# Performance work log

Hardware: AMD Instinct MI355X
Metric: run time of the kernel (lower is better)

## Reference

```python
import jax, jax.numpy as jnp
import numpy as np

DIM, HEADS, WIN, MLP_H = 768, 12, 14, 3072
B, H0, W0 = 8, 64, 64
N = H0 * W0
SCALE = (DIM // HEADS) ** -0.5
EPS = 1e-5


def setup_inputs():
    key = jax.random.key(0)
    ks = jax.random.split(key, 8)
    w = lambda k, shape: jax.random.normal(k, shape, jnp.float32) * 0.02
    return {
        "x": jax.random.normal(ks[0], (B, N, DIM), jnp.float32),
        "rel_pos_bias": jax.random.normal(ks[1], (HEADS, WIN * WIN, WIN * WIN), jnp.float32) * 0.1,
        "ln1_g": jnp.ones((DIM,), jnp.float32),
        "ln1_b": jnp.zeros((DIM,), jnp.float32),
        "qkv_w": w(ks[2], (3 * DIM, DIM)),
        "qkv_b": jnp.zeros((3 * DIM,), jnp.float32),
        "proj_w": w(ks[3], (DIM, DIM)),
        "proj_b": jnp.zeros((DIM,), jnp.float32),
        "ln2_g": jnp.ones((DIM,), jnp.float32),
        "ln2_b": jnp.zeros((DIM,), jnp.float32),
        "fc1_w": w(ks[4], (MLP_H, DIM)),
        "fc1_b": jnp.zeros((MLP_H,), jnp.float32),
        "fc2_w": w(ks[5], (DIM, MLP_H)),
        "fc2_b": jnp.zeros((DIM,), jnp.float32),
        "H": H0,
        "W": W0,
    }


def layernorm(x, g, b):
    m = x.mean(-1, keepdims=True)
    v = ((x - m) ** 2).mean(-1, keepdims=True)
    return (x - m) / jnp.sqrt(v + EPS) * g + b


def make_window(x, H, W, win):
    Bc, _, C = x.shape
    x = x.reshape(Bc, H, W, C)
    ph, pw = (-H) % win, (-W) % win
    x = jnp.pad(x, ((0, 0), (0, ph), (0, pw), (0, 0)))
    Hp, Wp = H + ph, W + pw
    x = x.reshape(Bc, Hp // win, win, Wp // win, win, C)
    x = x.transpose(0, 1, 3, 2, 4, 5).reshape(-1, win * win, C)
    return x, Hp, Wp


def revert_window(x, Hp, Wp, H, W, win):
    Bc = x.shape[0] // ((Hp // win) * (Wp // win))
    C = x.shape[-1]
    x = x.reshape(Bc, Hp // win, Wp // win, win, win, C)
    x = x.transpose(0, 1, 3, 2, 4, 5).reshape(Bc, Hp, Wp, C)
    return x[:, :H, :W, :].reshape(Bc, H * W, C)


def attention(x, rel_pos_bias, qkv_w, qkv_b, proj_w, proj_b):
    Bw, Nw, C = x.shape
    dh = C // HEADS
    qkv = (x @ qkv_w.T + qkv_b).reshape(Bw, Nw, 3, HEADS, dh)
    q, k, v = (qkv[:, :, i].transpose(0, 2, 1, 3) for i in range(3))  # [Bw, h, Nw, dh]
    attn = jnp.einsum("bhqd,bhkd->bhqk", q, k) * SCALE + rel_pos_bias[None]
    attn = jax.nn.softmax(attn, axis=-1)
    out = jnp.einsum("bhqk,bhkd->bhqd", attn, v)
    out = out.transpose(0, 2, 1, 3).reshape(Bw, Nw, C)
    return out @ proj_w.T + proj_b


def reference(x, rel_pos_bias, ln1_g, ln1_b, qkv_w, qkv_b, proj_w, proj_b,
              ln2_g, ln2_b, fc1_w, fc1_b, fc2_w, fc2_b, H, W):
    ori = x
    h = layernorm(x, ln1_g, ln1_b)
    hw, Hp, Wp = make_window(h, H, W, WIN)
    hw = attention(hw, rel_pos_bias, qkv_w, qkv_b, proj_w, proj_b)
    h = revert_window(hw, Hp, Wp, H, W, WIN)
    x = ori + h
    m = layernorm(x, ln2_g, ln2_b)
    m = jax.nn.gelu(m @ fc1_w.T + fc1_b, approximate=False) @ fc2_w.T + fc2_b
    return x + m
```

## Files before the change

### kernel.cpp

```cpp
#include <hip/hip_runtime.h>


typedef unsigned short u16;
typedef unsigned int u32;
typedef __attribute__((ext_vector_type(4))) float f32x4;
typedef __attribute__((ext_vector_type(8))) __bf16 bf16x8;

#define DIMC 768
#define HEADS 12
#define WIN2 196
#define MLP_H 3072
#define MW 39200
#define MWPAD 39296
#define HW_ROWS 39312
#define MM 32768

__device__ __forceinline__ u16 f2bf(float f) {
  u32 u = __float_as_uint(f);
  u32 r = (u + 0x7fffu + ((u >> 16) & 1u)) >> 16;
  return (u16)r;
}

__device__ __forceinline__ f32x4 mfma16(bf16x8 a, bf16x8 b, f32x4 c) {
  return __builtin_amdgcn_mfma_f32_16x16x32_bf16(a, b, c, 0, 0, 0);
}

__device__ __forceinline__ void gload_lds16(const u16* g, u16* l) {
  __builtin_amdgcn_global_load_lds((__attribute__((address_space(1))) void*)g,
                                   (__attribute__((address_space(3))) void*)l,
                                   16, 0, 0);
}

__global__ __launch_bounds__(256) void cvt_bf16(const float* __restrict__ s,
                                                u16* __restrict__ d, int n) {
  for (int i = blockIdx.x * 256 + threadIdx.x; i < n; i += gridDim.x * 256)
    d[i] = f2bf(s[i]);
}

__global__ __launch_bounds__(256) void ln1_win_kernel(const float* __restrict__ x,
    const float* __restrict__ g, const float* __restrict__ bb,
    u16* __restrict__ hw) {
  int row = blockIdx.x;
  int t = threadIdx.x;
  const float* src = nullptr;
  if (row < MW) {
    int w = row / WIN2, p = row % WIN2;
    int b = w / 25, wi = w % 25;
    int wy = wi / 5, wx = wi % 5;
    int yy = wy * 14 + p / 14, xx = wx * 14 + p % 14;
    if (yy < 64 && xx < 64) src = x + ((size_t)b * 4096 + (size_t)yy * 64 + xx) * DIMC;
  }
  u16* dst = hw + (size_t)row * DIMC;
  if (src == nullptr) {
    for (int i = t; i < DIMC; i += 256) dst[i] = 0;
    return;
  }
  float v0 = src[t], v1 = src[t + 256], v2 = src[t + 512];
  __shared__ float red[8];
  float s = v0 + v1 + v2;
#pragma unroll
  for (int o = 32; o >= 1; o >>= 1) s += __shfl_xor(s, o);
  if ((t & 63) == 0) red[t >> 6] = s;
  __syncthreads();
  float mean = (red[0] + red[1] + red[2] + red[3]) * (1.0f / 768.0f);
  float d0 = v0 - mean, d1 = v1 - mean, d2 = v2 - mean;
  float q = d0 * d0 + d1 * d1 + d2 * d2;
#pragma unroll
  for (int o = 32; o >= 1; o >>= 1) q += __shfl_xor(q, o);
  if ((t & 63) == 0) red[4 + (t >> 6)] = q;
  __syncthreads();
  float var = (red[4] + red[5] + red[6] + red[7]) * (1.0f / 768.0f);
  float rstd = rsqrtf(var + 1e-5f);
  dst[t]       = f2bf(d0 * rstd * g[t]       + bb[t]);
  dst[t + 256] = f2bf(d1 * rstd * g[t + 256] + bb[t + 256]);
  dst[t + 512] = f2bf(d2 * rstd * g[t + 512] + bb[t + 512]);
}

__global__ __launch_bounds__(256) void ln_kernel(const float* __restrict__ x,
    const float* __restrict__ g, const float* __restrict__ bb,
    u16* __restrict__ out) {
  int row = blockIdx.x;
  int t = threadIdx.x;
  const float* src = x + (size_t)row * DIMC;
  u16* dst = out + (size_t)row * DIMC;
  float v0 = src[t], v1 = src[t + 256], v2 = src[t + 512];
  __shared__ float red[8];
  float s = v0 + v1 + v2;
#pragma unroll
  for (int o = 32; o >= 1; o >>= 1) s += __shfl_xor(s, o);
  if ((t & 63) == 0) red[t >> 6] = s;
  __syncthreads();
  float mean = (red[0] + red[1] + red[2] + red[3]) * (1.0f / 768.0f);
  float d0 = v0 - mean, d1 = v1 - mean, d2 = v2 - mean;
  float q = d0 * d0 + d1 * d1 + d2 * d2;
#pragma unroll
  for (int o = 32; o >= 1; o >>= 1) q += __shfl_xor(q, o);
  if ((t & 63) == 0) red[4 + (t >> 6)] = q;
  __syncthreads();
  float var = (red[4] + red[5] + red[6] + red[7]) * (1.0f / 768.0f);
  float rstd = rsqrtf(var + 1e-5f);
  dst[t]       = f2bf(d0 * rstd * g[t]       + bb[t]);
  dst[t + 256] = f2bf(d1 * rstd * g[t + 256] + bb[t + 256]);
  dst[t + 512] = f2bf(d2 * rstd * g[t + 512] + bb[t + 512]);
}

template <int EPI>
__global__ __launch_bounds__(256) void gemm_bt(
    const u16* __restrict__ A, const u16* __restrict__ W,
    const float* __restrict__ bias, int K, int N,
    u16* __restrict__ outb, float* __restrict__ outf,
    const float* __restrict__ resid) {
  __shared__ u16 As[128 * 32];
  __shared__ u16 Bs[128 * 32];
  int tid = threadIdx.x, lane = tid & 63, wv = tid >> 6;
  int bm = blockIdx.x, bn = blockIdx.y;
  int wr = wv >> 1, wc = wv & 1;
  const int fq = lane >> 4, fr = lane & 15;

  f32x4 acc[4][4];
#pragma unroll
  for (int m = 0; m < 4; ++m)
#pragma unroll
    for (int n = 0; n < 4; ++n) acc[m][n] = f32x4{0.f, 0.f, 0.f, 0.f};

  int nk = K >> 5;
  for (int kt = 0; kt < nk; ++kt) {
#pragma unroll
    for (int s2 = 0; s2 < 2; ++s2) {
      int seg = wv * 2 + s2;
      int ci = seg * 64 + lane;
      int rowIn = ci >> 2;
      int kch = (ci & 3) ^ (rowIn & 3);
      const u16* ga = A + (size_t)(bm * 128 + rowIn) * K + kt * 32 + kch * 8;
      gload_lds16(ga, &As[seg * 512]);
      const u16* gb = W + (size_t)(bn * 128 + rowIn) * K + kt * 32 + kch * 8;
      gload_lds16(gb, &Bs[seg * 512]);
    }
    __syncthreads();
    bf16x8 af[4], bfr[4];
#pragma unroll
    for (int m = 0; m < 4; ++m) {
      int row = wr * 64 + m * 16 + fr;
      int kch = fq ^ (row & 3);
      af[m] = *(const bf16x8*)&As[row * 32 + kch * 8];
    }
#pragma unroll
    for (int n = 0; n < 4; ++n) {
      int row = wc * 64 + n * 16 + fr;
      int kch = fq ^ (row & 3);
      bfr[n] = *(const bf16x8*)&Bs[row * 32 + kch * 8];
    }
#pragma unroll
    for (int m = 0; m < 4; ++m)
#pragma unroll
      for (int n = 0; n < 4; ++n)
        acc[m][n] = mfma16(af[m], bfr[n], acc[m][n]);
    __syncthreads();
  }

  float bcol[4];
#pragma unroll
  for (int n = 0; n < 4; ++n) bcol[n] = bias[bn * 128 + wc * 64 + n * 16 + fr];

#pragma unroll
  for (int m = 0; m < 4; ++m) {
#pragma unroll
    for (int j = 0; j < 4; ++j) {
      int row = bm * 128 + wr * 64 + m * 16 + fq * 4 + j;
#pragma unroll
      for (int n = 0; n < 4; ++n) {
        int col = bn * 128 + wc * 64 + n * 16 + fr;
        float v = acc[m][n][j] + bcol[n];
        if constexpr (EPI == 0) {
          outb[(size_t)row * N + col] = f2bf(v);
        } else if constexpr (EPI == 2) {
          v = 0.5f * v * (1.0f + erff(v * 0.70710678118654752f));
          outb[(size_t)row * N + col] = f2bf(v);
        } else if constexpr (EPI == 1) {
          if (row < MW) {
            int w = row / WIN2, p = row % WIN2;
            int b = w / 25, wi = w % 25;
            int yy = (wi / 5) * 14 + p / 14, xx = (wi % 5) * 14 + p % 14;
            if (yy < 64 && xx < 64) {
              size_t o = ((size_t)b * 4096 + (size_t)yy * 64 + xx) * DIMC + col;
              outf[o] = resid[o] + v;
            }
          }
        } else {
          size_t o = (size_t)row * DIMC + col;
          outf[o] = resid[o] + v;
        }
      }
    }
  }
}

#define ATTN_LDS 94208
__global__ __launch_bounds__(256) void attn_kernel(const u16* __restrict__ qkv,
    const float* __restrict__ bias, u16* __restrict__ aout) {
  extern __shared__ char smem[];
  int tid = threadIdx.x, lane = tid & 63, wv = tid >> 6;
  int blk = blockIdx.x;
  int w = blk / HEADS, h = blk % HEADS;
  const size_t rbase = (size_t)w * WIN2;
  char* KsB = smem;
  char* VtB = smem + 28672;
  char* PsB = smem + 61440 + wv * 8192;

  for (int c = tid; c < 1792; c += 256) {
    int row = c >> 3, off = (c & 7) << 4;
    char* d = KsB + row * 128 + (off ^ ((row & 7) << 4));
    if (row < WIN2) {
      const u16* gp = qkv + (rbase + row) * 2304 + 768 + h * 64 + (off >> 1);
      *(uint4*)d = *(const uint4*)gp;
    } else {
      *(uint4*)d = make_uint4(0u, 0u, 0u, 0u);
    }
  }
  for (int c = tid; c < 1792; c += 256) {
    int row = c >> 3, d0 = (c & 7) << 3;
    u16 tmp[8];
    if (row < WIN2) {
      const u16* gp = qkv + (rbase + row) * 2304 + 1536 + h * 64 + d0;
#pragma unroll
      for (int i = 0; i < 8; ++i) tmp[i] = gp[i];
    } else {
#pragma unroll
      for (int i = 0; i < 8; ++i) tmp[i] = 0;
    }
#pragma unroll
    for (int i = 0; i < 8; ++i) {
      int dd = d0 + i;
      int k2 = row << 1;
      *(u16*)(VtB + dd * 512 + (k2 ^ ((dd & 7) << 4))) = tmp[i];
    }
  }
  __syncthreads();

  const int fq = lane >> 4, fr = lane & 15;
  for (int qt = wv; qt < 13; qt += 4) {
    int qrow = qt * 16 + fr;
    if (qrow > 195) qrow = 195;
    const u16* qg = qkv + (rbase + qrow) * 2304 + h * 64 + fq * 8;
    bf16x8 qa0 = *(const bf16x8*)qg;
    bf16x8 qa1 = *(const bf16x8*)(qg + 32);

    f32x4 sacc[14];
#pragma unroll
    for (int ct = 0; ct < 14; ++ct) {
      int krow = ct * 16 + fr;
      const char* kp = KsB + krow * 128;
      bf16x8 kb0 = *(const bf16x8*)(kp + ((fq * 16) ^ ((krow & 7) << 4)));
      bf16x8 kb1 = *(const bf16x8*)(kp + ((64 + fq * 16) ^ ((krow & 7) << 4)));
      f32x4 z = f32x4{0.f, 0.f, 0.f, 0.f};
      z = mfma16(qa0, kb0, z);
      z = mfma16(qa1, kb1, z);
      sacc[ct] = z;
    }

    int qb = qt * 16 + fq * 4;
    float rs[4];
#pragma unroll
    for (int j = 0; j < 4; ++j) {
      int q = qb + j;
      int qc = q > 195 ? 195 : q;
      const float* bp = bias + ((size_t)h * WIN2 + qc) * WIN2;
      float mx = -1e30f;
#pragma unroll
      for (int ct = 0; ct < 14; ++ct) {
        int kc = ct * 16 + fr;
        float sv = (kc < WIN2) ? sacc[ct][j] * 0.125f + bp[kc] : -1e30f;
        sacc[ct][j] = sv;
        mx = fmaxf(mx, sv);
      }
#pragma unroll
      for (int o = 1; o < 16; o <<= 1) mx = fmaxf(mx, __shfl_xor(mx, o));
      float sum = 0.f;
#pragma unroll
      for (int ct = 0; ct < 14; ++ct) {
        float p = __expf(sacc[ct][j] - mx);
        sacc[ct][j] = p;
        sum += p;
      }
#pragma unroll
      for (int o = 1; o < 16; o <<= 1) sum += __shfl_xor(sum, o);
      rs[j] = sum;
    }

#pragma unroll
    for (int ct = 0; ct < 14; ++ct) {
#pragma unroll
      for (int j = 0; j < 4; ++j) {
        int r = fq * 4 + j;
        int c2 = (ct * 16 + fr) << 1;
        *(u16*)(PsB + r * 512 + (c2 ^ ((r & 7) << 4))) = f2bf(sacc[ct][j]);
      }
    }
    asm volatile("s_waitcnt lgkmcnt(0)" ::: "memory");
    __builtin_amdgcn_sched_barrier(0);

    f32x4 oacc[4];
#pragma unroll
    for (int dt = 0; dt < 4; ++dt) oacc[dt] = f32x4{0.f, 0.f, 0.f, 0.f};
#pragma unroll
    for (int kt = 0; kt < 7; ++kt) {
      bf16x8 pa =
          *(const bf16x8*)(PsB + fr * 512 + ((kt * 64 + fq * 16) ^ ((fr & 7) << 4)));
#pragma unroll
      for (int dt = 0; dt < 4; ++dt) {
        int vd = dt * 16 + fr;
        bf16x8 vb =
            *(const bf16x8*)(VtB + vd * 512 + ((kt * 64 + fq * 16) ^ ((vd & 7) << 4)));
        oacc[dt] = mfma16(pa, vb, oacc[dt]);
      }
    }

#pragma unroll
    for (int j = 0; j < 4; ++j) {
      int q = qb + j;
      if (q < WIN2) {
        float inv = 1.0f / rs[j];
#pragma unroll
        for (int dt = 0; dt < 4; ++dt) {
          aout[(rbase + q) * DIMC + h * 64 + dt * 16 + fr] = f2bf(oacc[dt][j] * inv);
        }
      }
    }
  }
}

extern "C" void kernel_launch(void* const* d_in, const int* in_sizes, int n_in,
                              void* d_out, int out_size, void* d_ws, size_t ws_size,
                              hipStream_t stream) {
  const float* x      = (const float*)d_in[0];
  const float* rpb    = (const float*)d_in[1];
  const float* ln1_g  = (const float*)d_in[2];
  const float* ln1_b  = (const float*)d_in[3];
  const float* qkv_w  = (const float*)d_in[4];
  const float* qkv_b  = (const float*)d_in[5];
  const float* proj_w = (const float*)d_in[6];
  const float* proj_b = (const float*)d_in[7];
  const float* ln2_g  = (const float*)d_in[8];
  const float* ln2_b  = (const float*)d_in[9];
  const float* fc1_w  = (const float*)d_in[10];
  const float* fc1_b  = (const float*)d_in[11];
  const float* fc2_w  = (const float*)d_in[12];
  const float* fc2_b  = (const float*)d_in[13];
  float* out = (float*)d_out;

  char* ws = (char*)d_ws;
  const size_t W_QKV = (size_t)2304 * 768 * 2;
  const size_t W_PRJ = (size_t)768 * 768 * 2;
  const size_t W_FC1 = (size_t)3072 * 768 * 2;
  const size_t W_FC2 = (size_t)768 * 3072 * 2;
  const size_t WB = W_QKV + W_PRJ + W_FC1 + W_FC2;
  const size_t HWB = (size_t)HW_ROWS * DIMC * 2;
  u16* wqkv  = (u16*)ws;
  u16* wproj = (u16*)(ws + W_QKV);
  u16* wfc1  = (u16*)(ws + W_QKV + W_PRJ);
  u16* wfc2  = (u16*)(ws + W_QKV + W_PRJ + W_FC1);
  u16* hw    = (u16*)(ws + WB);
  u16* bufB  = (u16*)(ws + WB + HWB);

  int Cq = 0;
  const int cqs[4] = {1, 2, 4, 8};
  for (int t = 0; t < 4; ++t) {
    int cq = cqs[t];
    int rowsW = (200 / cq) * 196;
    size_t pr = (size_t)((rowsW + 127) / 128) * 128;
    size_t q_b = pr * 2304 * 2;
    size_t f_b = (size_t)(MM / cq) * MLP_H * 2;
    size_t bb = q_b > f_b ? q_b : f_b;
    if (WB + HWB + bb <= ws_size) { Cq = cq; break; }
  }
  if (Cq == 0) return;
  const int Cm = Cq;
  const int Wc = 200 / Cq;
  const int rowsW = Wc * 196;
  const int padRows = ((rowsW + 127) / 128) * 128;
  const int Rm = MM / Cm;

  cvt_bf16<<<2048, 256, 0, stream>>>(qkv_w, wqkv, 2304 * 768);
  cvt_bf16<<<2048, 256, 0, stream>>>(proj_w, wproj, 768 * 768);
  cvt_bf16<<<2048, 256, 0, stream>>>(fc1_w, wfc1, 3072 * 768);
  cvt_bf16<<<2048, 256, 0, stream>>>(fc2_w, wfc2, 768 * 3072);

  ln1_win_kernel<<<HW_ROWS, 256, 0, stream>>>(x, ln1_g, ln1_b, hw);

  hipFuncSetAttribute((const void*)attn_kernel,
                      hipFuncAttributeMaxDynamicSharedMemorySize, ATTN_LDS);
  for (int c = 0; c < Cq; ++c) {
    const u16* Ac = hw + (size_t)c * rowsW * DIMC;
    gemm_bt<0><<<dim3(padRows / 128, 2304 / 128), 256, 0, stream>>>(
        Ac, wqkv, qkv_b, 768, 2304, bufB, nullptr, nullptr);
    attn_kernel<<<Wc * HEADS, 256, ATTN_LDS, stream>>>(
        bufB, rpb, hw + (size_t)c * rowsW * DIMC);
  }

  gemm_bt<1><<<dim3(MWPAD / 128, DIMC / 128), 256, 0, stream>>>(
      hw, wproj, proj_b, 768, DIMC, nullptr, out, x);

  u16* ln2b = hw;
  ln_kernel<<<MM, 256, 0, stream>>>(out, ln2_g, ln2_b, ln2b);

  for (int m = 0; m < Cm; ++m) {
    gemm_bt<2><<<dim3(Rm / 128, MLP_H / 128), 256, 0, stream>>>(
        ln2b + (size_t)m * Rm * DIMC, wfc1, fc1_b, 768, MLP_H,
        bufB, nullptr, nullptr);
    float* outc = out + (size_t)m * Rm * DIMC;
    gemm_bt<3><<<dim3(Rm / 128, DIMC / 128), 256, 0, stream>>>(
        bufB, wfc2, fc2_b, 3072, DIMC, nullptr, outc, outc);
  }
}
```

Before: 1.410 ms.

## Replace GEMM with 256x256 double-buffered 8-wave pipelined MFMA kernel

Replaces the 128x128, single-stage, 4-wave GEMM with a 256x256 tile, 8-wave kernel using BK=64 and double-buffered LDS (128 KB dynamic). Global-to-LDS loads for the next tiles are interleaved with four MFMA quadrants, using explicit waitcnt, barriers and setprio to overlap memory with compute. Row padding grows to multiples of 256, with larger HW_ROWS and MWPAD. The goals are higher arithmetic intensity per tile and hiding load latency. The risks are fewer blocks for small N (the 768-wide GEMMs launch only 3 column tiles) and occupancy limits from 128 KB of LDS.

```diff
diff --git a/kernel.cpp b/kernel.cpp
--- a/kernel.cpp
+++ b/kernel.cpp
@@ -11,8 +11,8 @@
 #define WIN2 196
 #define MLP_H 3072
 #define MW 39200
-#define MWPAD 39296
-#define HW_ROWS 39312
+#define MWPAD 39424
+#define HW_ROWS 39424
 #define MM 32768
 
 __device__ __forceinline__ u16 f2bf(float f) {
@@ -104,73 +104,155 @@
   dst[t + 512] = f2bf(d2 * rstd * g[t + 512] + bb[t + 512]);
 }
 
+__device__ __forceinline__ void stageA8(const u16* __restrict__ G, int K,
+    int rowBase, int tile, u16* ldsM, int h, int wv, int lane) {
+#pragma unroll
+  for (int i = 0; i < 2; ++i) {
+    int o = (i * 8 + wv) * 8;
+    int rb = h * 64 + ((o < 64) ? o : (o + 64));
+    int r = rb + (lane >> 3);
+    int lc = (lane & 7) ^ (r & 7);
+    const u16* g = G + (size_t)(rowBase + r) * K + tile * 64 + lc * 8;
+    gload_lds16(g, ldsM + rb * 64);
+  }
+}
+__device__ __forceinline__ void stageB8(const u16* __restrict__ G, int K,
+    int rowBase, int tile, u16* ldsM, int h, int wv, int lane) {
+#pragma unroll
+  for (int i = 0; i < 2; ++i) {
+    int o = (i * 8 + wv) * 8;
+    int rb = (o >> 5) * 64 + h * 32 + (o & 31);
+    int r = rb + (lane >> 3);
+    int lc = (lane & 7) ^ (r & 7);
+    const u16* g = G + (size_t)(rowBase + r) * K + tile * 64 + lc * 8;
+    gload_lds16(g, ldsM + rb * 64);
+  }
+}
+__device__ __forceinline__ void readA8(const u16* lA, int wrM, int mh,
+    int fq, int fr, bf16x8 a[4][2]) {
+#pragma unroll
+  for (int mf2 = 0; mf2 < 4; ++mf2) {
+    int rt = wrM * 128 + mh * 64 + mf2 * 16 + fr;
+#pragma unroll
+    for (int kk = 0; kk < 2; ++kk) {
+      int c3 = (kk * 4 + fq) ^ (rt & 7);
+      a[mf2][kk] = *(const bf16x8*)(lA + rt * 64 + c3 * 8);
+    }
+  }
+}
+__device__ __forceinline__ void readB8(const u16* lB, int wcN, int nh,
+    int fq, int fr, bf16x8 b[2][2]) {
+#pragma unroll
+  for (int nf2 = 0; nf2 < 2; ++nf2) {
+    int rt = wcN * 64 + nh * 32 + nf2 * 16 + fr;
+#pragma unroll
+    for (int kk = 0; kk < 2; ++kk) {
+      int c3 = (kk * 4 + fq) ^ (rt & 7);
+      b[nf2][kk] = *(const bf16x8*)(lB + rt * 64 + c3 * 8);
+    }
+  }
+}
+
+#define MFMA_Q(MH, NH, AR, BR)                                             \
+  _Pragma("unroll") for (int mf2 = 0; mf2 < 4; ++mf2)                      \
+  _Pragma("unroll") for (int nf2 = 0; nf2 < 2; ++nf2)                      \
+  _Pragma("unroll") for (int kk = 0; kk < 2; ++kk)                         \
+    acc[(MH)*4 + mf2][(NH)*2 + nf2] =                                      \
+        mfma16(AR[mf2][kk], BR[nf2][kk], acc[(MH)*4 + mf2][(NH)*2 + nf2]);
+
 template <int EPI>
-__global__ __launch_bounds__(256) void gemm_bt(
+__global__ __launch_bounds__(512, 2) void gemm8(
     const u16* __restrict__ A, const u16* __restrict__ W,
     const float* __restrict__ bias, int K, int N,
     u16* __restrict__ outb, float* __restrict__ outf,
     const float* __restrict__ resid) {
-  __shared__ u16 As[128 * 32];
-  __shared__ u16 Bs[128 * 32];
+  extern __shared__ u16 lds[];
   int tid = threadIdx.x, lane = tid & 63, wv = tid >> 6;
   int bm = blockIdx.x, bn = blockIdx.y;
-  int wr = wv >> 1, wc = wv & 1;
-  const int fq = lane >> 4, fr = lane & 15;
-
-  f32x4 acc[4][4];
-#pragma unroll
-  for (int m = 0; m < 4; ++m)
-#pragma unroll
-    for (int n = 0; n < 4; ++n) acc[m][n] = f32x4{0.f, 0.f, 0.f, 0.f};
-
-  int nk = K >> 5;
-  for (int kt = 0; kt < nk; ++kt) {
-#pragma unroll
-    for (int s2 = 0; s2 < 2; ++s2) {
-      int seg = wv * 2 + s2;
-      int ci = seg * 64 + lane;
-      int rowIn = ci >> 2;
-      int kch = (ci & 3) ^ (rowIn & 3);
-      const u16* ga = A + (size_t)(bm * 128 + rowIn) * K + kt * 32 + kch * 8;
-      gload_lds16(ga, &As[seg * 512]);
-      const u16* gb = W + (size_t)(bn * 128 + rowIn) * K + kt * 32 + kch * 8;
-      gload_lds16(gb, &Bs[seg * 512]);
-    }
-    __syncthreads();
-    bf16x8 af[4], bfr[4];
-#pragma unroll
-    for (int m = 0; m < 4; ++m) {
-      int row = wr * 64 + m * 16 + fr;
-      int kch = fq ^ (row & 3);
-      af[m] = *(const bf16x8*)&As[row * 32 + kch * 8];
-    }
-#pragma unroll
-    for (int n = 0; n < 4; ++n) {
-      int row = wc * 64 + n * 16 + fr;
-      int kch = fq ^ (row & 3);
-      bfr[n] = *(const bf16x8*)&Bs[row * 32 + kch * 8];
-    }
-#pragma unroll
-    for (int m = 0; m < 4; ++m)
-#pragma unroll
-      for (int n = 0; n < 4; ++n)
-        acc[m][n] = mfma16(af[m], bfr[n], acc[m][n]);
-    __syncthreads();
+  int wrM = wv >> 2, wcN = wv & 3;
+  int fq = lane >> 4, fr = lane & 15;
+  int rowBase = bm * 256, colBase = bn * 256;
+  int nk = K >> 6;
+
+  f32x4 acc[8][4];
+#pragma unroll
+  for (int i = 0; i < 8; ++i)
+#pragma unroll
+    for (int j = 0; j < 4; ++j) acc[i][j] = f32x4{0.f, 0.f, 0.f, 0.f};
+
+  u16* A0d = lds;
+  u16* B0d = lds + 16384;
+  u16* A1d = lds + 32768;
+  u16* B1d = lds + 49152;
+
+  stageA8(A, K, rowBase, 0, A0d, 0, wv, lane);
+  stageB8(W, K, colBase, 0, B0d, 0, wv, lane);
+  stageB8(W, K, colBase, 0, B0d, 1, wv, lane);
+  stageA8(A, K, rowBase, 0, A0d, 1, wv, lane);
+  stageA8(A, K, rowBase, 1, A1d, 0, wv, lane);
+  stageB8(W, K, colBase, 1, B1d, 0, wv, lane);
+  stageB8(W, K, colBase, 1, B1d, 1, wv, lane);
+
+  bf16x8 a[4][2], b0[2][2], b1[2][2];
+
+  for (int T = 0; T < nk; ++T) {
+    u16* lA = lds + (T & 1) * 32768;
+    u16* lB = lA + 16384;
+    u16* lAo = lds + ((T + 1) & 1) * 32768;
+
+    if (T == nk - 1) { asm volatile("s_waitcnt vmcnt(0)" ::: "memory"); }
+    else             { asm volatile("s_waitcnt vmcnt(6)" ::: "memory"); }
+    __builtin_amdgcn_s_barrier();
+    __builtin_amdgcn_sched_barrier(0);
+
+    readA8(lA, wrM, 0, fq, fr, a);
+    readB8(lB, wcN, 0, fq, fr, b0);
+    if (T + 1 < nk) stageA8(A, K, rowBase, T + 1, lAo, 1, wv, lane);
+    asm volatile("s_waitcnt lgkmcnt(0)" ::: "memory");
+    __builtin_amdgcn_sched_barrier(0);
+    __builtin_amdgcn_s_setprio(1);
+    MFMA_Q(0, 0, a, b0)
+    __builtin_amdgcn_s_setprio(0);
+    __builtin_amdgcn_s_barrier();
+
+    readB8(lB, wcN, 1, fq, fr, b1);
+    if (T + 2 < nk) stageA8(A, K, rowBase, T + 2, lA, 0, wv, lane);
+    asm volatile("s_waitcnt lgkmcnt(0)" ::: "memory");
+    __builtin_amdgcn_sched_barrier(0);
+    __builtin_amdgcn_s_setprio(1);
+    MFMA_Q(0, 1, a, b1)
+    __builtin_amdgcn_s_setprio(0);
+    __builtin_amdgcn_s_barrier();
+
+    readA8(lA, wrM, 1, fq, fr, a);
+    if (T + 2 < nk) stageB8(W, K, colBase, T + 2, lB, 0, wv, lane);
+    asm volatile("s_waitcnt lgkmcnt(0)" ::: "memory");
+    __builtin_amdgcn_sched_barrier(0);
+    __builtin_amdgcn_s_setprio(1);
+    MFMA_Q(1, 1, a, b1)
+    __builtin_amdgcn_s_setprio(0);
+    __builtin_amdgcn_s_barrier();
+
+    if (T + 2 < nk) stageB8(W, K, colBase, T + 2, lB, 1, wv, lane);
+    __builtin_amdgcn_s_setprio(1);
+    MFMA_Q(1, 0, a, b0)
+    __builtin_amdgcn_s_setprio(0);
   }
 
   float bcol[4];
 #pragma unroll
-  for (int n = 0; n < 4; ++n) bcol[n] = bias[bn * 128 + wc * 64 + n * 16 + fr];
-
-#pragma unroll
-  for (int m = 0; m < 4; ++m) {
+  for (int nf = 0; nf < 4; ++nf)
+    bcol[nf] = bias[colBase + wcN * 64 + nf * 16 + fr];
+
+#pragma unroll
+  for (int mf = 0; mf < 8; ++mf) {
 #pragma unroll
     for (int j = 0; j < 4; ++j) {
-      int row = bm * 128 + wr * 64 + m * 16 + fq * 4 + j;
-#pragma unroll
-      for (int n = 0; n < 4; ++n) {
-        int col = bn * 128 + wc * 64 + n * 16 + fr;
-        float v = acc[m][n][j] + bcol[n];
+      int row = rowBase + wrM * 128 + mf * 16 + fq * 4 + j;
+#pragma unroll
+      for (int nf = 0; nf < 4; ++nf) {
+        int col = colBase + wcN * 64 + nf * 16 + fr;
+        float v = acc[mf][nf][j] + bcol[nf];
         if constexpr (EPI == 0) {
           outb[(size_t)row * N + col] = f2bf(v);
         } else if constexpr (EPI == 2) {
@@ -366,8 +448,8 @@
   const int cqs[4] = {1, 2, 4, 8};
   for (int t = 0; t < 4; ++t) {
     int cq = cqs[t];
-    int rowsW = (200 / cq) * 196;
-    size_t pr = (size_t)((rowsW + 127) / 128) * 128;
+    int rw = (200 / cq) * 196;
+    size_t pr = (size_t)((rw + 255) / 256) * 256;
     size_t q_b = pr * 2304 * 2;
     size_t f_b = (size_t)(MM / cq) * MLP_H * 2;
     size_t bb = q_b > f_b ? q_b : f_b;
@@ -377,7 +459,7 @@
   const int Cm = Cq;
   const int Wc = 200 / Cq;
   const int rowsW = Wc * 196;
-  const int padRows = ((rowsW + 127) / 128) * 128;
+  const int padRows = ((rowsW + 255) / 256) * 256;
   const int Rm = MM / Cm;
 
   cvt_bf16<<<2048, 256, 0, stream>>>(qkv_w, wqkv, 2304 * 768);
@@ -387,28 +469,37 @@
 
   ln1_win_kernel<<<HW_ROWS, 256, 0, stream>>>(x, ln1_g, ln1_b, hw);
 
+  hipFuncSetAttribute((const void*)gemm8<0>,
+                      hipFuncAttributeMaxDynamicSharedMemorySize, 131072);
+  hipFuncSetAttribute((const void*)gemm8<1>,
+                      hipFuncAttributeMaxDynamicSharedMemorySize, 131072);
+  hipFuncSetAttribute((const void*)gemm8<2>,
+                      hipFuncAttributeMaxDynamicSharedMemorySize, 131072);
+  hipFuncSetAttribute((const void*)gemm8<3>,
+                      hipFuncAttributeMaxDynamicSharedMemorySize, 131072);
   hipFuncSetAttribute((const void*)attn_kernel,
                       hipFuncAttributeMaxDynamicSharedMemorySize, ATTN_LDS);
+
   for (int c = 0; c < Cq; ++c) {
     const u16* Ac = hw + (size_t)c * rowsW * DIMC;
-    gemm_bt<0><<<dim3(padRows / 128, 2304 / 128), 256, 0, stream>>>(
+    gemm8<0><<<dim3(padRows / 256, 2304 / 256), 512, 131072, stream>>>(
         Ac, wqkv, qkv_b, 768, 2304, bufB, nullptr, nullptr);
     attn_kernel<<<Wc * HEADS, 256, ATTN_LDS, stream>>>(
         bufB, rpb, hw + (size_t)c * rowsW * DIMC);
   }
 
-  gemm_bt<1><<<dim3(MWPAD / 128, DIMC / 128), 256, 0, stream>>>(
+  gemm8<1><<<dim3(MWPAD / 256, DIMC / 256), 512, 131072, stream>>>(
       hw, wproj, proj_b, 768, DIMC, nullptr, out, x);
 
   u16* ln2b = hw;
   ln_kernel<<<MM, 256, 0, stream>>>(out, ln2_g, ln2_b, ln2b);
 
   for (int m = 0; m < Cm; ++m) {
-    gemm_bt<2><<<dim3(Rm / 128, MLP_H / 128), 256, 0, stream>>>(
+    gemm8<2><<<dim3(Rm / 256, MLP_H / 256), 512, 131072, stream>>>(
         ln2b + (size_t)m * Rm * DIMC, wfc1, fc1_b, 768, MLP_H,
         bufB, nullptr, nullptr);
     float* outc = out + (size_t)m * Rm * DIMC;
-    gemm_bt<3><<<dim3(Rm / 128, DIMC / 128), 256, 0, stream>>>(
+    gemm8<3><<<dim3(Rm / 256, DIMC / 256), 512, 131072, stream>>>(
         bufB, wfc2, fc2_b, 3072, DIMC, nullptr, outc, outc);
   }
 }
```

Measured after the change: 1.279 ms. -9.3%, faster.
